# Kernel tuning notes

Measured on AMD Instinct MI355X. Metric: run time of the kernel, lower is better.

## Reference

```python
import jax, jax.numpy as jnp
import numpy as np

N, E, D, H, C = 50000, 250000, 300, 4, 75  # nodes, edges, in_size=300, heads=4, out=75 (H*C=300)


def setup_inputs() -> dict:
    key = jax.random.key(0)
    ks = jax.random.split(key, 32)
    rn = lambda k, shape, s=0.05: jax.random.normal(k, shape, jnp.float32) * s
    inp = {}
    inp['x'] = rn(ks[0], (N, D), 1.0)
    inp['edge_index'] = jax.random.randint(ks[1], (2, E), 0, N, dtype=jnp.int32)
    inp['edge_attr'] = rn(ks[2], (E, 4), 1.0)
    inp['obj_normals'] = rn(ks[3], (N, 3), 1.0)
    # parameters (Linear stored as [in, out] so y = x @ W + b)
    inp['Wq'] = rn(ks[4], (D, H * C)); inp['bq'] = rn(ks[5], (H * C,))
    inp['Wk'] = rn(ks[6], (D, H * C)); inp['bk'] = rn(ks[7], (H * C,))
    inp['Wv'] = rn(ks[8], (D, H * C)); inp['bv'] = rn(ks[9], (H * C,))
    inp['We'] = rn(ks[10], (D, H * C))               # lin_edge, no bias
    inp['Wn'] = rn(ks[11], (3, D)); inp['bn'] = rn(ks[12], (D,))      # map_normal
    inp['Wxy'] = rn(ks[13], (2, D)); inp['bxy'] = rn(ks[14], (D,))    # map_xy_relative_coord
    inp['Wloc'] = rn(ks[15], (3 * D, D)); inp['bloc'] = rn(ks[16], (D,))  # map_back_edge_loc
    inp['Wobj'] = rn(ks[17], (2 * D, D)); inp['bobj'] = rn(ks[18], (D,))  # map_back_edge_obj
    inp['Wfus'] = rn(ks[19], (2 * D, D)); inp['bfus'] = rn(ks[20], (D,))  # hv_words_fusion
    inp['Wcls'] = rn(ks[21], (D, 5)); inp['bcls'] = rn(ks[22], (5,))      # horizontal_word_cls
    inp['Wskip'] = rn(ks[23], (D, H * C)); inp['bskip'] = rn(ks[24], (H * C,))  # lin_skip
    inp['vocab'] = rn(ks[25], (7, D), 1.0)  # spatial_vocab_we
    return inp


def reference(x, edge_index, edge_attr, obj_normals,
              Wq, bq, Wk, bk, Wv, bv, We, Wn, bn, Wxy, bxy,
              Wloc, bloc, Wobj, bobj, Wfus, bfus, Wcls, bcls,
              Wskip, bskip, vocab):
    src, dst = edge_index[0], edge_index[1]  # x_j = x[src], x_i = x[dst]
    x_i = x[dst]
    x_j = x[src]
    q = (x_i @ Wq + bq).reshape(E, H, C)
    k = (x_j @ Wk + bk).reshape(E, H, C)
    # vertical (top/bottom) word embeddings gated by edge_attr signs
    top = (edge_attr[:, 0] > 0).astype(x.dtype)[:, None] * vocab[0][None, :]
    bot = (edge_attr[:, 1] < 0).astype(x.dtype)[:, None] * vocab[1][None, :]
    vert = top + bot                                           # [E, D]
    # horizontal word probabilities from geometry + feature cues
    ni = obj_normals[dst] @ Wn + bn
    nj = obj_normals[src] @ Wn + bn
    xy = edge_attr[:, 2:4] @ Wxy + bxy
    loc = jnp.concatenate([xy, ni, nj], axis=1) @ Wloc + bloc
    obj = jnp.concatenate([x_i, x_j - x_i], axis=1) @ Wobj + bobj
    prob = jax.nn.softmax(jnp.tanh(obj + loc) @ Wcls + bcls, axis=1)   # [E, 5]
    horiz = prob @ vocab[2:7]                                  # [E, D]
    edge_word = jnp.concatenate([vert, horiz], axis=1) @ Wfus + bfus   # [E, D]
    ef = (edge_word @ We).reshape(E, H, C)                     # lin_edge
    k = k + ef
    # scaled dot-product attention with per-destination-node softmax
    alpha = (q * k).sum(-1) / jnp.asarray(np.sqrt(C), x.dtype)  # [E, H]
    m = jax.ops.segment_max(alpha, dst, num_segments=N)
    alpha = jnp.exp(alpha - m[dst])
    den = jax.ops.segment_sum(alpha, dst, num_segments=N)
    alpha = alpha / den[dst]
    v = (x_j @ Wv + bv).reshape(E, H, C) + ef
    msg = v * alpha[..., None]                                  # [E, H, C]
    out = jax.ops.segment_sum(msg, dst, num_segments=N).reshape(N, H * C)
    out = out + x @ Wskip + bskip                               # concat heads + root skip
    return out
```

## Files before the change

kernel.cpp:

```cpp
#include <hip/hip_runtime.h>
#include <hip/hip_bf16.h>
#include <math.h>

#define NDIM 300
#define KPAD 320
#define NREAL 1800
#define NPAD 1920

typedef __hip_bfloat16 bf16;
typedef __attribute__((ext_vector_type(8))) short short8;
typedef __attribute__((ext_vector_type(4))) float f32x4;

__device__ __forceinline__ void gl_lds16(const void* g, void* l) {
    __builtin_amdgcn_global_load_lds(
        (const __attribute__((address_space(1))) void*)g,
        (__attribute__((address_space(3))) void*)l, 16, 0, 0);
}

__device__ __forceinline__ float bflo(uint u) { return __uint_as_float(u << 16); }
__device__ __forceinline__ float bfhi(uint u) { return __uint_as_float(u & 0xFFFF0000u); }

__global__ void k1_pre_conv_hist(
    const float* __restrict__ Wn, const float* __restrict__ bn,
    const float* __restrict__ Wxy, const float* __restrict__ bxy,
    const float* __restrict__ Wloc, const float* __restrict__ bloc,
    const float* __restrict__ bobj,
    const float* __restrict__ Wfus,
    const float* __restrict__ vocab,
    float* __restrict__ Wn1, float* __restrict__ Wn2,
    float* __restrict__ Mxy, float* __restrict__ bgeo,
    float* __restrict__ vf5, float* __restrict__ t0, float* __restrict__ t1,
    const float* __restrict__ X, const float* __restrict__ Nrm,
    bf16* __restrict__ Xb, int M, int nconv,
    const int* __restrict__ ei, int* __restrict__ deg, int E)
{
    const int bid = blockIdx.x;
    if (bid < 19) {
        int i = bid * 256 + threadIdx.x;
        if (i < 900) {
            int r = i / 300, c = i % 300;
            float s = 0.f;
            for (int k = 0; k < 300; k++) s += Wn[r*300+k] * Wloc[(300+k)*300+c];
            Wn1[i] = s;
        } else if (i < 1800) {
            int j = i - 900; int r = j/300, c = j%300;
            float s = 0.f;
            for (int k = 0; k < 300; k++) s += Wn[r*300+k] * Wloc[(600+k)*300+c];
            Wn2[j] = s;
        } else if (i < 2400) {
            int j = i - 1800; int r = j/300, c = j%300;
            float s = 0.f;
            for (int k = 0; k < 300; k++) s += Wxy[r*300+k] * Wloc[k*300+c];
            Mxy[j] = 2.f * s;
        } else if (i < 2700) {
            int c = i - 2400;
            float s = bloc[c] + bobj[c];
            for (int k = 0; k < 300; k++) s += bxy[k] * Wloc[k*300+c];
            for (int k = 0; k < 300; k++) s += bn[k] * (Wloc[(300+k)*300+c] + Wloc[(600+k)*300+c]);
            bgeo[c] = 2.f * s;
        } else if (i < 4200) {
            int j = i - 2700; int p = j/300, c = j%300;
            float s = 0.f;
            for (int k = 0; k < 300; k++) s += vocab[(2+p)*300+k] * Wfus[(300+k)*300+c];
            vf5[j] = s;
        } else if (i < 4500) {
            int c = i - 4200;
            float s = 0.f;
            for (int k = 0; k < 300; k++) s += vocab[k] * Wfus[k*300+c];
            t0[c] = s;
        } else if (i < 4800) {
            int c = i - 4500;
            float s = 0.f;
            for (int k = 0; k < 300; k++) s += vocab[300+k] * Wfus[k*300+c];
            t1[c] = s;
        }
    } else if (bid < 19 + nconv) {
        int i = (bid - 19) * 256 + threadIdx.x;
        int row = i / 40, c8 = i % 40;
        if (row >= M) return;
        int c0 = c8 * 8;
        union { bf16 h[8]; short8 s; } u;
        #pragma unroll
        for (int t = 0; t < 8; t++) {
            int c = c0 + t;
            float v = 0.f;
            if (c < 300)      v = X[(size_t)row * 300 + c];
            else if (c < 303) v = Nrm[(size_t)row * 3 + (c - 300)];
            u.h[t] = __float2bfloat16(v);
        }
        *(short8*)&Xb[(size_t)row * 320 + c0] = u.s;
    } else {
        int e = (bid - 19 - nconv) * 256 + threadIdx.x;
        if (e < E) atomicAdd(&deg[ei[E + e]], 1);
    }
}

__global__ void k2_pre2_pack(
    const float* __restrict__ We, const float* __restrict__ bfus,
    const float* __restrict__ vf5, const float* __restrict__ t0, const float* __restrict__ t1,
    const float* __restrict__ Wcls,
    float* __restrict__ E8, float* __restrict__ WclsT,
    const float* __restrict__ Wq, const float* __restrict__ Wk,
    const float* __restrict__ Wv, const float* __restrict__ Wskip,
    const float* __restrict__ Wobj,
    const float* __restrict__ Wn1, const float* __restrict__ Wn2,
    const float* __restrict__ bq, const float* __restrict__ bk,
    const float* __restrict__ bv, const float* __restrict__ bskip,
    bf16* __restrict__ WcatT, float* __restrict__ bcat)
{
    const int bid = blockIdx.x;
    if (bid < 16) {
        int i = bid * 256 + threadIdx.x;
        if (i < 2400) {
            int r = i / 300, c = i % 300;
            const float* src;
            if (r == 0) src = t0;
            else if (r == 1) src = t1;
            else if (r == 7) src = bfus;
            else src = vf5 + (r - 2) * 300;
            float s = 0.f;
            for (int k = 0; k < 300; k++) s += src[k] * We[k*300+c];
            E8[i] = s;
        } else if (i < 3900) {
            int j = i - 2400; int cl = j / 300, c = j % 300;
            WclsT[cl * 300 + c] = Wcls[c * 5 + cl];
        }
    } else {
        int i = (bid - 16) * 256 + threadIdx.x;
        if (i < NREAL) {
            int c = i;
            float b = 0.f;
            if (c < 600)       { if (!(c & 1)) b = bq[c >> 1]; }
            else if (c < 1200) { int cc = c - 600; if (cc & 1) b = bk[cc >> 1]; }
            else if (c < 1500) b = bv[c - 1200];
            else               b = bskip[c - 1500];
            bcat[i] = b;
        }
        if (i < NPAD * KPAD) {
            int cp = i / KPAD, k = i % KPAD;
            float v = 0.f;
            if (cp < NREAL) {
                int seg, jj;
                if (cp < 600)       { jj = cp >> 1; seg = (cp & 1) ? 4 : 0; }
                else if (cp < 1200) { int cc = cp - 600; jj = cc >> 1; seg = (cc & 1) ? 1 : 5; }
                else if (cp < 1500) { jj = cp - 1200; seg = 2; }
                else                { jj = cp - 1500; seg = 3; }
                if (k < 300) {
                    switch (seg) {
                        case 0: v = Wq[k*300+jj]; break;
                        case 1: v = Wk[k*300+jj]; break;
                        case 2: v = Wv[k*300+jj]; break;
                        case 3: v = Wskip[k*300+jj]; break;
                        case 4: v = Wobj[k*300+jj] - Wobj[(300+k)*300+jj]; break;
                        default: v = Wobj[(300+k)*300+jj]; break;
                    }
                } else if (k < 303) {
                    if (seg == 4) v = Wn1[(k-300)*300+jj];
                    else if (seg == 5) v = Wn2[(k-300)*300+jj];
                }
                if (seg >= 4) v *= 2.f;
            }
            WcatT[i] = __float2bfloat16(v);
        }
    }
}

__global__ __launch_bounds__(1024) void scan_local(
    const int* __restrict__ deg, int* __restrict__ off, int* __restrict__ bsum, int N)
{
    __shared__ int buf[1024];
    int i = blockIdx.x * 1024 + threadIdx.x;
    int v = (i < N) ? deg[i] : 0;
    buf[threadIdx.x] = v;
    __syncthreads();
    #pragma unroll
    for (int ofs = 1; ofs < 1024; ofs <<= 1) {
        int t = (threadIdx.x >= ofs) ? buf[threadIdx.x - ofs] : 0;
        __syncthreads();
        buf[threadIdx.x] += t;
        __syncthreads();
    }
    if (i < N) off[i] = buf[threadIdx.x] - v;
    if (threadIdx.x == 1023) bsum[blockIdx.x] = buf[1023];
}

__global__ __launch_bounds__(1024) void scan_bsum(
    const int* __restrict__ bsum, int* __restrict__ bexc, int nb)
{
    __shared__ int buf[1024];
    int v = (threadIdx.x < nb) ? bsum[threadIdx.x] : 0;
    buf[threadIdx.x] = v;
    __syncthreads();
    #pragma unroll
    for (int ofs = 1; ofs < 1024; ofs <<= 1) {
        int t = (threadIdx.x >= ofs) ? buf[threadIdx.x - ofs] : 0;
        __syncthreads();
        buf[threadIdx.x] += t;
        __syncthreads();
    }
    if (threadIdx.x < nb) bexc[threadIdx.x] = buf[threadIdx.x] - v;
}

__global__ void scan_add(int* __restrict__ off, int* __restrict__ cur,
                         const int* __restrict__ bexc, int N, int E)
{
    int i = blockIdx.x * blockDim.x + threadIdx.x;
    if (i < N) {
        int o = off[i] + bexc[i >> 10];
        off[i] = o; cur[i] = o;
    }
    if (i == 0) off[N] = E;
}

__global__ __launch_bounds__(256) void gemm_mfma(
    const bf16* __restrict__ Xb,
    const bf16* __restrict__ Bt, const float* __restrict__ bcat,
    bf16* __restrict__ QP, bf16* __restrict__ PK, bf16* __restrict__ V,
    float* __restrict__ Ot, int M, int npan)
{
    __shared__ __align__(16) char smraw[32768];
    bf16*  Asb = (bf16*)smraw;
    bf16*  Bsb = (bf16*)(smraw + 16384);
    bf16*  EP  = (bf16*)smraw;
    float* EPf = (float*)smraw;

    const int bid = blockIdx.x;
    int p, cx;
    {
        const int full = (npan >> 3) * 120;
        if (bid < full) {
            int g = bid / 120, r = bid - g * 120;
            p = (g << 3) + (r & 7); cx = r >> 3;
        } else {
            int r = bid - full;
            int tp = npan & 7;
            p = (npan & ~7) + r % tp; cx = r / tp;
        }
    }
    const int r0 = p * 128;
    const int c0 = cx * 128;

    const int tid  = threadIdx.x;
    const int wave = tid >> 6;
    const int lane = tid & 63;
    const int wm = (wave >> 1) * 64;
    const int wn = (wave & 1) * 64;
    const int lr = lane & 15;
    const int lq = lane >> 4;

    f32x4 acc[4][4];
    #pragma unroll
    for (int j = 0; j < 4; j++)
        #pragma unroll
        for (int i = 0; i < 4; i++) acc[j][i] = (f32x4){0.f, 0.f, 0.f, 0.f};

    const bf16* aSrc[2];
    const bf16* bSrc[2];
    {
        const int bcol_l = lane >> 2;
        const int bkp    = (lane & 3) * 8;
        #pragma unroll
        for (int h = 0; h < 2; h++) {
            int t = h * 256 + wave * 64 + lane;
            int grow = min(r0 + (t >> 2), M - 1);
            aSrc[h] = Xb + (size_t)grow * 320 + (t & 3) * 8;
            bSrc[h] = Bt + (size_t)(c0 + wave * 32 + h * 16 + bcol_l) * KPAD + bkp;
        }
    }

    auto stage = [&](int buf, int kb) {
        #pragma unroll
        for (int h = 0; h < 2; h++) {
            int tbase = h * 256 + wave * 64;
            gl_lds16(aSrc[h] + kb, &Asb[buf * 4096 + tbase * 8]);
        }
        #pragma unroll
        for (int h = 0; h < 2; h++) {
            int cloc = wave * 32 + h * 16;
            gl_lds16(bSrc[h] + kb, &Bsb[buf * 4096 + cloc * 32]);
        }
    };

    stage(0, 0);
    #pragma unroll
    for (int it = 0; it < 10; it++) {
        __syncthreads();
        if (it < 9) stage((it + 1) & 1, (it + 1) * 32);
        const int b = it & 1;
        short8 af[4], bfr[4];
        #pragma unroll
        for (int i = 0; i < 4; i++)
            af[i] = *(const short8*)&Asb[b * 4096 + (wm + i * 16 + lr) * 32 + lq * 8];
        #pragma unroll
        for (int j = 0; j < 4; j++)
            bfr[j] = *(const short8*)&Bsb[b * 4096 + (wn + j * 16 + lr) * 32 + lq * 8];
        #pragma unroll
        for (int j = 0; j < 4; j++)
            #pragma unroll
            for (int i = 0; i < 4; i++)
                acc[j][i] = __builtin_amdgcn_mfma_f32_16x16x32_bf16(
                    bfr[j], af[i], acc[j][i], 0, 0, 0);
    }

    if (c0 < 1500) {
        #pragma unroll
        for (int hm = 0; hm < 2; hm++) {
            __syncthreads();
            if ((wave >> 1) == hm) {
                #pragma unroll
                for (int j = 0; j < 4; j++) {
                    int colL = wn + j * 16 + lq * 4;
                    float4 bb = *(const float4*)&bcat[c0 + colL];
                    #pragma unroll
                    for (int i = 0; i < 4; i++) {
                        int row = i * 16 + lr;
                        union { bf16 h[4]; uint2 u2; } pk;
                        pk.h[0] = __float2bfloat16(acc[j][i][0] + bb.x);
                        pk.h[1] = __float2bfloat16(acc[j][i][1] + bb.y);
                        pk.h[2] = __float2bfloat16(acc[j][i][2] + bb.z);
                        pk.h[3] = __float2bfloat16(acc[j][i][3] + bb.w);
                        *(uint2*)&EP[row * 136 + colL] = pk.u2;
                    }
                }
            }
            __syncthreads();
            #pragma unroll
            for (int rep = 0; rep < 8; rep++) {
                int row = wave * 16 + rep * 2 + (lane >> 5);
                int gr = r0 + hm * 64 + row;
                int col = c0 + 4 * (lane & 31);
                if (gr < M && col < 1500) {
                    uint2 val = *(const uint2*)&EP[row * 136 + 4 * (lane & 31)];
                    if (col < 600)       *(uint2*)&QP[(size_t)gr * 600 + col] = val;
                    else if (col < 1200) *(uint2*)&PK[(size_t)gr * 600 + (col - 600)] = val;
                    else                 *(uint2*)&V [(size_t)gr * 300 + (col - 1200)] = val;
                }
            }
        }
    }
    if (c0 + 128 > 1500) {
        #pragma unroll
        for (int hm = 0; hm < 2; hm++) {
            #pragma unroll
            for (int h = 0; h < 2; h++) {
                if (c0 + h * 64 + 63 < 1500) continue;
                __syncthreads();
                if ((wave >> 1) == hm && (wave & 1) == h) {
                    #pragma unroll
                    for (int j = 0; j < 4; j++) {
                        int colL = j * 16 + lq * 4;
                        int colb = c0 + h * 64 + colL;
                        if (colb < NREAL) {
                            float4 bb = *(const float4*)&bcat[colb];
                            #pragma unroll
                            for (int i = 0; i < 4; i++) {
                                int row = i * 16 + lr;
                                f32x4 vv;
                                vv[0] = acc[j][i][0] + bb.x;
                                vv[1] = acc[j][i][1] + bb.y;
                                vv[2] = acc[j][i][2] + bb.z;
                                vv[3] = acc[j][i][3] + bb.w;
                                *(f32x4*)&EPf[row * 68 + colL] = vv;
                            }
                        }
                    }
                }
                __syncthreads();
                #pragma unroll
                for (int rep = 0; rep < 16; rep++) {
                    int row = wave * 16 + rep;
                    int gr = r0 + hm * 64 + row;
                    int col = c0 + h * 64 + lane;
                    if (gr < M && col >= 1500 && col < NREAL)
                        Ot[(size_t)gr * 300 + (col - 1500)] = EPf[row * 68 + lane];
                }
            }
        }
    }
}

__global__ __launch_bounds__(256) void k3_scatter_qe8(
    const int* __restrict__ ei, const float* __restrict__ ea,
    int* __restrict__ cur,
    int2* __restrict__ esd, float* __restrict__ eas, int E, int ebk,
    const bf16* __restrict__ QP, const float* __restrict__ E8,
    float* __restrict__ QE8f, int N)
{
    __shared__ unsigned short Qs[64 * 302];
    const int bid = blockIdx.x;
    if (bid < ebk) {
        int e = bid * 256 + threadIdx.x;
        if (e < E) {
            int s = ei[e];
            int d = ei[E + e];
            float4 a = *(const float4*)&ea[(size_t)e * 4];
            int p = atomicAdd(&cur[d], 1);
            esd[p] = make_int2(s, d);
            *(float4*)&eas[(size_t)p * 4] = a;
        }
        return;
    }
    const int tid = threadIdx.x;
    const int n0 = (bid - ebk) * 64;
    const int nrows = min(64, N - n0);
    const int nu = nrows * 300;
    const uint* src = (const uint*)QP + (size_t)n0 * 300;
    for (int i = tid; i < nu; i += 256) {
        int rr = i / 300, cc = i - rr * 300;
        Qs[rr * 302 + cc] = (unsigned short)src[i];
    }
    __syncthreads();
    const int w = tid >> 6, l = tid & 63;
    if (l >= nrows) return;
    float acc[8] = {0.f,0.f,0.f,0.f,0.f,0.f,0.f,0.f};
    const int cb = 75 * w;
    for (int cc = 0; cc < 75; cc++) {
        int c = cb + cc;
        float qv = __uint_as_float(((uint)Qs[l * 302 + c]) << 16);
        #pragma unroll
        for (int s = 0; s < 8; s++) acc[s] += qv * E8[s * 300 + c];
    }
    float* out = QE8f + (size_t)(n0 + l) * 32;
    #pragma unroll
    for (int s = 0; s < 8; s++) out[s * 4 + w] = acc[s];
}

__global__ __launch_bounds__(256) void edge_alpha(
    const int2* __restrict__ esd, const float* __restrict__ eas,
    const bf16* __restrict__ QP, const bf16* __restrict__ PK,
    const float* __restrict__ Mxy, const float* __restrict__ bgeo,
    const float* __restrict__ QE8f, const float* __restrict__ WclsT,
    const float* __restrict__ bcls,
    float* __restrict__ AW,
    int E, int nwaves)
{
    __shared__ __align__(16) float red[4][20 * 68];
    __shared__ float res[4][20];
    const int wv   = threadIdx.x >> 6;
    const int lane = threadIdx.x & 63;
    float* __restrict__ rw = red[wv];
    float* __restrict__ rs = res[wv];
    const int gw  = blockIdx.x * 4 + wv;
    const int per = (E + nwaves - 1) / nwaves;
    const int t0  = gw * per;
    if (t0 >= E) return;
    const int t1 = min(t0 + per, E);
    const bool ok4 = lane < 44;

    float mx0[5], mx1[5], bg[5], wcl[5][5];
    #pragma unroll
    for (int r = 0; r < 4; r++) {
        int c = lane + 64 * r;
        mx0[r] = Mxy[c]; mx1[r] = Mxy[300 + c]; bg[r] = bgeo[c];
        #pragma unroll
        for (int cl = 0; cl < 5; cl++) wcl[cl][r] = WclsT[cl * 300 + c];
    }
    {
        int c = lane + 256;
        mx0[4] = ok4 ? Mxy[c] : 0.f;
        mx1[4] = ok4 ? Mxy[300 + c] : 0.f;
        bg[4]  = ok4 ? bgeo[c] : 0.f;
        #pragma unroll
        for (int cl = 0; cl < 5; cl++) wcl[cl][4] = ok4 ? WclsT[cl * 300 + c] : 0.f;
    }
    float bc[5];
    #pragma unroll
    for (int cl = 0; cl < 5; cl++) bc[cl] = bcls[cl];
    const float isc = 0.11547005383792516f;

    const uint* QPu = (const uint*)QP;
    const uint* PKu = (const uint*)PK;

    int prev_d = -1;
    float qv[5], pib[5];
    float prt[18];

    auto reload = [&](int dd) {
        const uint* qr = QPu + (size_t)dd * 300 + lane;
        #pragma unroll
        for (int r = 0; r < 4; r++) {
            uint uq = qr[64 * r];
            qv[r] = bflo(uq); pib[r] = bfhi(uq) + bg[r];
        }
        uint uq = ok4 ? qr[256] : 0u;
        qv[4] = bflo(uq); pib[4] = bfhi(uq) + bg[4];
    };
    auto compute = [&](const uint (&pk)[5], float az, float aw_, int ub) {
        float tt[5], qk[5];
        #pragma unroll
        for (int r = 0; r < 5; r++) {
            float pj = bflo(pk[r]), kf = bfhi(pk[r]);
            float v = pib[r] + pj + az * mx0[r] + aw_ * mx1[r];
            tt[r] = fmaf(-2.f, __builtin_amdgcn_rcpf(1.f + __expf(v)), 1.f);
            qk[r] = qv[r] * kf;
        }
        #pragma unroll
        for (int cl = 0; cl < 5; cl++)
            prt[ub + cl] = tt[0]*wcl[cl][0] + tt[1]*wcl[cl][1] + tt[2]*wcl[cl][2]
                         + tt[3]*wcl[cl][3] + tt[4]*wcl[cl][4];
        float h0 = qk[0], h3 = qk[4], h1 = 0.f, h2 = 0.f;
        if (lane < 11) h0 += qk[1]; else h1 += qk[1];
        if (lane < 22) h1 += qk[2]; else h2 += qk[2];
        if (lane < 33) h2 += qk[3]; else h3 += qk[3];
        prt[ub+5] = h0; prt[ub+6] = h1; prt[ub+7] = h2; prt[ub+8] = h3;
    };

    for (int t = t0; t < t1; t += 2) {
        const int i0 = t;
        const int i1 = (t + 1 < t1) ? t + 1 : t;
        const int2 sd0 = esd[i0], sd1 = esd[i1];
        const float4 a40 = *(const float4*)&eas[(size_t)4 * i0];
        const float4 a41 = *(const float4*)&eas[(size_t)4 * i1];

        uint pk0[5], pk1[5];
        const uint* p0r = PKu + (size_t)sd0.x * 300 + lane;
        const uint* p1r = PKu + (size_t)sd1.x * 300 + lane;
        #pragma unroll
        for (int r = 0; r < 4; r++) { pk0[r] = p0r[64 * r]; pk1[r] = p1r[64 * r]; }
        pk0[4] = ok4 ? p0r[256] : 0u;
        pk1[4] = ok4 ? p1r[256] : 0u;

        if (sd0.y != prev_d) reload(sd0.y);
        compute(pk0, a40.z, a40.w, 0);
        if (sd1.y != sd0.y) reload(sd1.y);
        compute(pk1, a41.z, a41.w, 9);
        prev_d = sd1.y;

        #pragma unroll
        for (int v = 0; v < 18; v++) rw[v * 68 + lane] = prt[v];
        #pragma unroll
        for (int i = 0; i < 5; i++) {
            int v = 4 * i + (lane >> 4);
            const f32x4 q4 = *(const f32x4*)&rw[v * 68 + (lane & 15) * 4];
            float s = (q4[0] + q4[1]) + (q4[2] + q4[3]);
            s += __shfl_xor(s, 1, 64);
            s += __shfl_xor(s, 2, 64);
            s += __shfl_xor(s, 4, 64);
            s += __shfl_xor(s, 8, 64);
            if ((lane & 15) == 0 && v < 18) rs[v] = s;
        }
        {
            const int    u  = lane >> 5;
            const int    ub = u * 9;
            const float4 au = u ? a41 : a40;
            const int    dd = u ? sd1.y : sd0.y;
            const int    tw = u ? i1 : i0;
            float lg0 = rs[ub+0] + bc[0], lg1 = rs[ub+1] + bc[1], lg2 = rs[ub+2] + bc[2];
            float lg3 = rs[ub+3] + bc[3], lg4 = rs[ub+4] + bc[4];
            float mxv = fmaxf(fmaxf(fmaxf(lg0, lg1), fmaxf(lg2, lg3)), lg4);
            float p0 = __expf(lg0 - mxv), p1 = __expf(lg1 - mxv), p2 = __expf(lg2 - mxv);
            float p3 = __expf(lg3 - mxv), p4 = __expf(lg4 - mxv);
            float pinv = __builtin_amdgcn_rcpf(p0 + p1 + p2 + p3 + p4);
            p0 *= pinv; p1 *= pinv; p2 *= pinv; p3 *= pinv; p4 *= pinv;
            float ct  = au.x > 0.f ? 1.f : 0.f;
            float cb_ = au.y < 0.f ? 1.f : 0.f;
            const f32x4* qe = (const f32x4*)(QE8f + (size_t)dd * 32);
            f32x4 addv = ct*qe[0] + cb_*qe[1] + p0*qe[2] + p1*qe[3]
                       + p2*qe[4] + p3*qe[5] + p4*qe[6] + qe[7];
            float ax0 = __expf((rs[ub+5] + addv[0]) * isc);
            float ax1 = __expf((rs[ub+6] + addv[1]) * isc);
            float ax2 = __expf((rs[ub+7] + addv[2]) * isc);
            float ax3 = __expf((rs[ub+8] + addv[3]) * isc);
            if ((lane & 31) == 0) {
                float* awp = AW + (size_t)12 * tw;
                *(float4*)(awp)     = make_float4(ax0, ax1, ax2, ax3);
                *(float4*)(awp + 4) = make_float4(ct, cb_, p0, p1);
                *(float4*)(awp + 8) = make_float4(p2, p3, p4, 0.f);
            }
        }
    }
}

__global__ __launch_bounds__(256) void node_pv(
    const int2* __restrict__ esd, const bf16* __restrict__ V,
    const float* __restrict__ E8, const float* __restrict__ AW,
    const int* __restrict__ off,
    float* __restrict__ Ot, int N)
{
    const int wid  = threadIdx.x >> 6;
    const int lane = threadIdx.x & 63;
    const int n = blockIdx.x * 4 + wid;
    if (n >= N) return;
    const int e0 = off[n], e1 = off[n + 1];
    if (e0 == e1) return;
    const size_t nrow = (size_t)n * 300;
    const bool ok4 = lane < 44;

    float e8r[8][5];
    #pragma unroll
    for (int rr = 0; rr < 8; rr++) {
        #pragma unroll
        for (int r = 0; r < 4; r++) e8r[rr][r] = E8[rr * 300 + lane + 64 * r];
        e8r[rr][4] = ok4 ? E8[rr * 300 + lane + 256] : 0.f;
    }

    float macc[5] = {0.f, 0.f, 0.f, 0.f, 0.f};
    float den0 = 0.f, den1 = 0.f, den2 = 0.f, den3 = 0.f;

    int t = e0;
    for (; t + 4 <= e1; t += 4) {
        int s4[4];
        #pragma unroll
        for (int u = 0; u < 4; u++) s4[u] = esd[t + u].x;
        float vv[4][5];
        #pragma unroll
        for (int u = 0; u < 4; u++) {
            const bf16* vr = V + (size_t)s4[u] * 300 + lane;
            #pragma unroll
            for (int r = 0; r < 4; r++) vv[u][r] = __bfloat162float(vr[64 * r]);
            vv[u][4] = ok4 ? __bfloat162float(vr[256]) : 0.f;
        }
        #pragma unroll
        for (int u = 0; u < 4; u++) {
            const float* awp = AW + (size_t)12 * (t + u);
            float4 ax = *(const float4*)(awp);
            float4 wa = *(const float4*)(awp + 4);
            float4 wb = *(const float4*)(awp + 8);
            #pragma unroll
            for (int r = 0; r < 5; r++) {
                float efc = wa.x * e8r[0][r] + wa.y * e8r[1][r] + wa.z * e8r[2][r]
                          + wa.w * e8r[3][r] + wb.x * e8r[4][r] + wb.y * e8r[5][r]
                          + wb.z * e8r[6][r] + e8r[7][r];
                float w = (r == 0) ? ax.x
                        : (r == 1) ? (lane < 11 ? ax.x : ax.y)
                        : (r == 2) ? (lane < 22 ? ax.y : ax.z)
                        : (r == 3) ? (lane < 33 ? ax.z : ax.w)
                        : ax.w;
                macc[r] += w * (vv[u][r] + efc);
            }
            den0 += ax.x; den1 += ax.y; den2 += ax.z; den3 += ax.w;
        }
    }
    for (; t < e1; t++) {
        int s = esd[t].x;
        const float* awp = AW + (size_t)12 * t;
        float4 ax = *(const float4*)(awp);
        float4 wa = *(const float4*)(awp + 4);
        float4 wb = *(const float4*)(awp + 8);
        const bf16* vr = V + (size_t)s * 300 + lane;
        #pragma unroll
        for (int r = 0; r < 5; r++) {
            float vvs = (r < 4) ? __bfloat162float(vr[64 * r])
                                : (ok4 ? __bfloat162float(vr[256]) : 0.f);
            float efc = wa.x * e8r[0][r] + wa.y * e8r[1][r] + wa.z * e8r[2][r]
                      + wa.w * e8r[3][r] + wb.x * e8r[4][r] + wb.y * e8r[5][r]
                      + wb.z * e8r[6][r] + e8r[7][r];
            float w = (r == 0) ? ax.x
                    : (r == 1) ? (lane < 11 ? ax.x : ax.y)
                    : (r == 2) ? (lane < 22 ? ax.y : ax.z)
                    : (r == 3) ? (lane < 33 ? ax.z : ax.w)
                    : ax.w;
            macc[r] += w * (vvs + efc);
        }
        den0 += ax.x; den1 += ax.y; den2 += ax.z; den3 += ax.w;
    }

    const float rd0 = __builtin_amdgcn_rcpf(den0);
    const float rd1 = __builtin_amdgcn_rcpf(den1);
    const float rd2 = __builtin_amdgcn_rcpf(den2);
    const float rd3 = __builtin_amdgcn_rcpf(den3);
    #pragma unroll
    for (int r = 0; r < 5; r++) {
        int c = lane + 64 * r;
        if (c < 300) {
            float rd = (r == 0) ? rd0
                     : (r == 1) ? (lane < 11 ? rd0 : rd1)
                     : (r == 2) ? (lane < 22 ? rd1 : rd2)
                     : (r == 3) ? (lane < 33 ? rd2 : rd3)
                     : rd3;
            Ot[nrow + c] += macc[r] * rd;
        }
    }
}

extern "C" void kernel_launch(void* const* d_in, const int* in_sizes, int n_in,
                              void* d_out, int out_size, void* d_ws, size_t ws_size,
                              hipStream_t stream)
{
    const float* x     = (const float*)d_in[0];
    const int*   ei    = (const int*)  d_in[1];
    const float* ea    = (const float*)d_in[2];
    const float* on    = (const float*)d_in[3];
    const float* Wq    = (const float*)d_in[4];
    const float* bq    = (const float*)d_in[5];
    const float* Wk    = (const float*)d_in[6];
    const float* bk    = (const float*)d_in[7];
    const float* Wv    = (const float*)d_in[8];
    const float* bv    = (const float*)d_in[9];
    const float* We    = (const float*)d_in[10];
    const float* Wn    = (const float*)d_in[11];
    const float* bn    = (const float*)d_in[12];
    const float* Wxy   = (const float*)d_in[13];
    const float* bxy   = (const float*)d_in[14];
    const float* Wloc  = (const float*)d_in[15];
    const float* bloc  = (const float*)d_in[16];
    const float* Wobj  = (const float*)d_in[17];
    const float* bobj  = (const float*)d_in[18];
    const float* Wfus  = (const float*)d_in[19];
    const float* bfus  = (const float*)d_in[20];
    const float* Wcls  = (const float*)d_in[21];
    const float* bcls  = (const float*)d_in[22];
    const float* Wskip = (const float*)d_in[23];
    const float* bskip = (const float*)d_in[24];
    const float* vocab = (const float*)d_in[25];

    const int N = in_sizes[0] / NDIM;
    const int E = in_sizes[1] / 2;

    const size_t nodeElems = (size_t)N * 300;
    const size_t wcatElems = (size_t)NPAD * KPAD;
    const size_t xbElems   = (size_t)N * 320;
    size_t xbBytes = xbElems * sizeof(bf16);
    const size_t ovlBytes = ((size_t)16 * E + (size_t)32 * N) * sizeof(float);
    if (ovlBytes > xbBytes) xbBytes = ovlBytes;

    const size_t f32Elems  = NREAL + 904 + 904 + 600 + 304 + 1504 + 304 + 304 + 2400 + 1504;
    const size_t intElems  = (size_t)N + (size_t)(N + 1) + (size_t)N
                           + (size_t)2 * E + 2048;
    size_t need = (5 * nodeElems + wcatElems) * sizeof(bf16) + xbBytes
                + f32Elems * sizeof(float) + intElems * sizeof(int);
    if (ws_size < need) return;

    bf16* wsh = (bf16*)d_ws;
    bf16* QPb   = wsh;
    bf16* PKb   = QPb + (size_t)2 * nodeElems;
    bf16* Vb    = PKb + (size_t)2 * nodeElems;
    bf16* WcatT = Vb + nodeElems;
    bf16* Xb    = WcatT + wcatElems;
    float* AW   = (float*)Xb;
    float* eas  = AW + (size_t)12 * E;
    float* QE8f = eas + (size_t)4 * E;
    float* ws = (float*)((char*)Xb + xbBytes);
    size_t o = 0;
    float* bcat  = ws + o; o += NREAL;
    float* Wn1   = ws + o; o += 904;
    float* Wn2   = ws + o; o += 904;
    float* Mxyb  = ws + o; o += 600;
    float* bgeo  = ws + o; o += 304;
    float* vf5   = ws + o; o += 1504;
    float* t0b   = ws + o; o += 304;
    float* t1b   = ws + o; o += 304;
    float* E8b   = ws + o; o += 2400;
    float* WclsT = ws + o; o += 1504;
    int* ip = (int*)(ws + o);
    int* deg    = ip;             ip += N;
    int* offb   = ip;             ip += N + 1;
    int* curb   = ip;             ip += N;
    int2* esd   = (int2*)ip;      ip += (size_t)2 * E;
    int* bsum   = ip;             ip += 1024;
    int* bexc   = ip;             ip += 1024;
    (void)n_in; (void)out_size;

    hipMemsetAsync(deg, 0, (size_t)N * sizeof(int), stream);

    const int ebk   = (E + 255) / 256;
    const int nconv = ((int)((size_t)N * 40) + 255) / 256;

    k1_pre_conv_hist<<<19 + nconv + ebk, 256, 0, stream>>>(
        Wn, bn, Wxy, bxy, Wloc, bloc, bobj, Wfus, vocab,
        Wn1, Wn2, Mxyb, bgeo, vf5, t0b, t1b,
        x, on, Xb, N, nconv, ei, deg, E);
    k2_pre2_pack<<<16 + (NPAD * KPAD + 255) / 256, 256, 0, stream>>>(
        We, bfus, vf5, t0b, t1b, Wcls, E8b, WclsT,
        Wq, Wk, Wv, Wskip, Wobj, Wn1, Wn2, bq, bk, bv, bskip, WcatT, bcat);

    const int nbl = (N + 1023) / 1024;
    scan_local<<<nbl, 1024, 0, stream>>>(deg, offb, bsum, N);
    scan_bsum<<<1, 1024, 0, stream>>>(bsum, bexc, nbl);
    scan_add<<<(N + 255) / 256, 256, 0, stream>>>(offb, curb, bexc, N, E);

    const int npan = (N + 127) / 128;
    gemm_mfma<<<npan * 15, 256, 0, stream>>>(Xb, WcatT, bcat,
                                             QPb, PKb, Vb, (float*)d_out, N, npan);

    k3_scatter_qe8<<<ebk + (N + 63) / 64, 256, 0, stream>>>(
        ei, ea, curb, esd, eas, E, ebk, QPb, E8b, QE8f, N);

    const int eab = 2048;
    edge_alpha<<<eab, 256, 0, stream>>>(esd, eas, QPb, PKb,
                                        Mxyb, bgeo, QE8f, WclsT, bcls,
                                        AW, E, eab * 4);

    const int nb = (N + 3) / 4;
    node_pv<<<nb, 256, 0, stream>>>(esd, Vb, E8b, AW,
                                    offb, (float*)d_out, N);
}
```

Baseline: 618.7 us.

## Fuse edge attention and node aggregation into one destination-partitioned kernel

Merges the per-edge alpha kernel and the per-node PV aggregation kernel into one kernel. Each wave binary-searches the CSR offsets to own a contiguous range of destination nodes, computes the attention weights for their edges and accumulates V messages at once. Per-edge weights pass through LDS instead of a global AW buffer, which removes a global write/read round trip and a kernel launch. Work balance now follows node boundaries, so skewed degree distributions can leave some waves with more edges, and a node spanning a chunk boundary is handled entirely by one wave.

```diff
diff --git a/kernel.cpp b/kernel.cpp
--- a/kernel.cpp
+++ b/kernel.cpp
@@ -425,35 +425,49 @@
     for (int s = 0; s < 8; s++) out[s * 4 + w] = acc[s];
 }
 
-__global__ __launch_bounds__(256) void edge_alpha(
+__global__ __launch_bounds__(256) void edge_fused(
     const int2* __restrict__ esd, const float* __restrict__ eas,
     const bf16* __restrict__ QP, const bf16* __restrict__ PK,
+    const bf16* __restrict__ V,
     const float* __restrict__ Mxy, const float* __restrict__ bgeo,
     const float* __restrict__ QE8f, const float* __restrict__ WclsT,
-    const float* __restrict__ bcls,
-    float* __restrict__ AW,
-    int E, int nwaves)
-{
-    __shared__ __align__(16) float red[4][20 * 68];
+    const float* __restrict__ bcls, const float* __restrict__ E8,
+    const int* __restrict__ off,
+    float* __restrict__ Ot, int N, int E, int nwaves)
+{
+    __shared__ __align__(16) float red[4][18 * 68];
     __shared__ float res[4][20];
+    __shared__ __align__(16) float ews[4][2][12];
     const int wv   = threadIdx.x >> 6;
     const int lane = threadIdx.x & 63;
     float* __restrict__ rw = red[wv];
     float* __restrict__ rs = res[wv];
+    float* __restrict__ ew = &ews[wv][0][0];
     const int gw  = blockIdx.x * 4 + wv;
     const int per = (E + nwaves - 1) / nwaves;
-    const int t0  = gw * per;
-    if (t0 >= E) return;
-    const int t1 = min(t0 + per, E);
+    const int lo  = gw * per;
+    if (lo >= E) return;
+    const int hi = min(lo + per, E);
+    int n0, n1;
+    {
+        int a = 0, b = N;
+        while (a < b) { int m = (a + b) >> 1; if (off[m] < lo) a = m + 1; else b = m; }
+        n0 = a; b = N;
+        while (a < b) { int m = (a + b) >> 1; if (off[m] < hi) a = m + 1; else b = m; }
+        n1 = a;
+    }
+    if (n0 >= n1) return;
     const bool ok4 = lane < 44;
 
-    float mx0[5], mx1[5], bg[5], wcl[5][5];
+    float mx0[5], mx1[5], bg[5], wcl[5][5], e8r[8][5];
     #pragma unroll
     for (int r = 0; r < 4; r++) {
         int c = lane + 64 * r;
         mx0[r] = Mxy[c]; mx1[r] = Mxy[300 + c]; bg[r] = bgeo[c];
         #pragma unroll
         for (int cl = 0; cl < 5; cl++) wcl[cl][r] = WclsT[cl * 300 + c];
+        #pragma unroll
+        for (int rr = 0; rr < 8; rr++) e8r[rr][r] = E8[rr * 300 + c];
     }
     {
         int c = lane + 256;
@@ -462,6 +476,8 @@
         bg[4]  = ok4 ? bgeo[c] : 0.f;
         #pragma unroll
         for (int cl = 0; cl < 5; cl++) wcl[cl][4] = ok4 ? WclsT[cl * 300 + c] : 0.f;
+        #pragma unroll
+        for (int rr = 0; rr < 8; rr++) e8r[rr][4] = ok4 ? E8[rr * 300 + c] : 0.f;
     }
     float bc[5];
     #pragma unroll
@@ -470,22 +486,10 @@
 
     const uint* QPu = (const uint*)QP;
     const uint* PKu = (const uint*)PK;
-
-    int prev_d = -1;
-    float qv[5], pib[5];
     float prt[18];
 
-    auto reload = [&](int dd) {
-        const uint* qr = QPu + (size_t)dd * 300 + lane;
-        #pragma unroll
-        for (int r = 0; r < 4; r++) {
-            uint uq = qr[64 * r];
-            qv[r] = bflo(uq); pib[r] = bfhi(uq) + bg[r];
-        }
-        uint uq = ok4 ? qr[256] : 0u;
-        qv[4] = bflo(uq); pib[4] = bfhi(uq) + bg[4];
-    };
-    auto compute = [&](const uint (&pk)[5], float az, float aw_, int ub) {
+    auto compute = [&](const uint (&pk)[5], const float (&qv)[5], const float (&pib)[5],
+                       float az, float aw_, int ub) {
         float tt[5], qk[5];
         #pragma unroll
         for (int r = 0; r < 5; r++) {
@@ -505,170 +509,134 @@
         prt[ub+5] = h0; prt[ub+6] = h1; prt[ub+7] = h2; prt[ub+8] = h3;
     };
 
-    for (int t = t0; t < t1; t += 2) {
-        const int i0 = t;
-        const int i1 = (t + 1 < t1) ? t + 1 : t;
-        const int2 sd0 = esd[i0], sd1 = esd[i1];
-        const float4 a40 = *(const float4*)&eas[(size_t)4 * i0];
-        const float4 a41 = *(const float4*)&eas[(size_t)4 * i1];
-
-        uint pk0[5], pk1[5];
-        const uint* p0r = PKu + (size_t)sd0.x * 300 + lane;
-        const uint* p1r = PKu + (size_t)sd1.x * 300 + lane;
-        #pragma unroll
-        for (int r = 0; r < 4; r++) { pk0[r] = p0r[64 * r]; pk1[r] = p1r[64 * r]; }
-        pk0[4] = ok4 ? p0r[256] : 0u;
-        pk1[4] = ok4 ? p1r[256] : 0u;
-
-        if (sd0.y != prev_d) reload(sd0.y);
-        compute(pk0, a40.z, a40.w, 0);
-        if (sd1.y != sd0.y) reload(sd1.y);
-        compute(pk1, a41.z, a41.w, 9);
-        prev_d = sd1.y;
-
-        #pragma unroll
-        for (int v = 0; v < 18; v++) rw[v * 68 + lane] = prt[v];
-        #pragma unroll
-        for (int i = 0; i < 5; i++) {
-            int v = 4 * i + (lane >> 4);
-            const f32x4 q4 = *(const f32x4*)&rw[v * 68 + (lane & 15) * 4];
-            float s = (q4[0] + q4[1]) + (q4[2] + q4[3]);
-            s += __shfl_xor(s, 1, 64);
-            s += __shfl_xor(s, 2, 64);
-            s += __shfl_xor(s, 4, 64);
-            s += __shfl_xor(s, 8, 64);
-            if ((lane & 15) == 0 && v < 18) rs[v] = s;
-        }
+    for (int n = n0; n < n1; n++) {
+        const int e0 = off[n], e1 = off[n + 1];
+        if (e0 == e1) continue;
+        float qv[5], pib[5];
         {
-            const int    u  = lane >> 5;
-            const int    ub = u * 9;
-            const float4 au = u ? a41 : a40;
-            const int    dd = u ? sd1.y : sd0.y;
-            const int    tw = u ? i1 : i0;
-            float lg0 = rs[ub+0] + bc[0], lg1 = rs[ub+1] + bc[1], lg2 = rs[ub+2] + bc[2];
-            float lg3 = rs[ub+3] + bc[3], lg4 = rs[ub+4] + bc[4];
-            float mxv = fmaxf(fmaxf(fmaxf(lg0, lg1), fmaxf(lg2, lg3)), lg4);
-            float p0 = __expf(lg0 - mxv), p1 = __expf(lg1 - mxv), p2 = __expf(lg2 - mxv);
-            float p3 = __expf(lg3 - mxv), p4 = __expf(lg4 - mxv);
-            float pinv = __builtin_amdgcn_rcpf(p0 + p1 + p2 + p3 + p4);
-            p0 *= pinv; p1 *= pinv; p2 *= pinv; p3 *= pinv; p4 *= pinv;
-            float ct  = au.x > 0.f ? 1.f : 0.f;
-            float cb_ = au.y < 0.f ? 1.f : 0.f;
-            const f32x4* qe = (const f32x4*)(QE8f + (size_t)dd * 32);
-            f32x4 addv = ct*qe[0] + cb_*qe[1] + p0*qe[2] + p1*qe[3]
-                       + p2*qe[4] + p3*qe[5] + p4*qe[6] + qe[7];
-            float ax0 = __expf((rs[ub+5] + addv[0]) * isc);
-            float ax1 = __expf((rs[ub+6] + addv[1]) * isc);
-            float ax2 = __expf((rs[ub+7] + addv[2]) * isc);
-            float ax3 = __expf((rs[ub+8] + addv[3]) * isc);
-            if ((lane & 31) == 0) {
-                float* awp = AW + (size_t)12 * tw;
-                *(float4*)(awp)     = make_float4(ax0, ax1, ax2, ax3);
-                *(float4*)(awp + 4) = make_float4(ct, cb_, p0, p1);
-                *(float4*)(awp + 8) = make_float4(p2, p3, p4, 0.f);
-            }
-        }
-    }
-}
-
-__global__ __launch_bounds__(256) void node_pv(
-    const int2* __restrict__ esd, const bf16* __restrict__ V,
-    const float* __restrict__ E8, const float* __restrict__ AW,
-    const int* __restrict__ off,
-    float* __restrict__ Ot, int N)
-{
-    const int wid  = threadIdx.x >> 6;
-    const int lane = threadIdx.x & 63;
-    const int n = blockIdx.x * 4 + wid;
-    if (n >= N) return;
-    const int e0 = off[n], e1 = off[n + 1];
-    if (e0 == e1) return;
-    const size_t nrow = (size_t)n * 300;
-    const bool ok4 = lane < 44;
-
-    float e8r[8][5];
-    #pragma unroll
-    for (int rr = 0; rr < 8; rr++) {
-        #pragma unroll
-        for (int r = 0; r < 4; r++) e8r[rr][r] = E8[rr * 300 + lane + 64 * r];
-        e8r[rr][4] = ok4 ? E8[rr * 300 + lane + 256] : 0.f;
-    }
-
-    float macc[5] = {0.f, 0.f, 0.f, 0.f, 0.f};
-    float den0 = 0.f, den1 = 0.f, den2 = 0.f, den3 = 0.f;
-
-    int t = e0;
-    for (; t + 4 <= e1; t += 4) {
-        int s4[4];
-        #pragma unroll
-        for (int u = 0; u < 4; u++) s4[u] = esd[t + u].x;
-        float vv[4][5];
-        #pragma unroll
-        for (int u = 0; u < 4; u++) {
-            const bf16* vr = V + (size_t)s4[u] * 300 + lane;
+            const uint* qr = QPu + (size_t)n * 300 + lane;
             #pragma unroll
-            for (int r = 0; r < 4; r++) vv[u][r] = __bfloat162float(vr[64 * r]);
-            vv[u][4] = ok4 ? __bfloat162float(vr[256]) : 0.f;
-        }
-        #pragma unroll
-        for (int u = 0; u < 4; u++) {
-            const float* awp = AW + (size_t)12 * (t + u);
-            float4 ax = *(const float4*)(awp);
-            float4 wa = *(const float4*)(awp + 4);
-            float4 wb = *(const float4*)(awp + 8);
+            for (int r = 0; r < 4; r++) {
+                uint uq = qr[64 * r];
+                qv[r] = bflo(uq); pib[r] = bfhi(uq) + bg[r];
+            }
+            uint uq = ok4 ? qr[256] : 0u;
+            qv[4] = bflo(uq); pib[4] = bfhi(uq) + bg[4];
+        }
+        const f32x4* qe = (const f32x4*)(QE8f + (size_t)n * 32);
+        float macc[5] = {0.f, 0.f, 0.f, 0.f, 0.f};
+        float den0 = 0.f, den1 = 0.f, den2 = 0.f, den3 = 0.f;
+
+        for (int t = e0; t < e1; t += 2) {
+            const int i0 = t;
+            const bool has1 = (t + 1 < e1);
+            const int i1 = has1 ? t + 1 : t;
+            const int s0 = esd[i0].x, s1 = esd[i1].x;
+            const float4 a40 = *(const float4*)&eas[(size_t)4 * i0];
+            const float4 a41 = *(const float4*)&eas[(size_t)4 * i1];
+
+            uint pk0[5], pk1[5];
+            const uint* p0r = PKu + (size_t)s0 * 300 + lane;
+            const uint* p1r = PKu + (size_t)s1 * 300 + lane;
             #pragma unroll
-            for (int r = 0; r < 5; r++) {
-                float efc = wa.x * e8r[0][r] + wa.y * e8r[1][r] + wa.z * e8r[2][r]
-                          + wa.w * e8r[3][r] + wb.x * e8r[4][r] + wb.y * e8r[5][r]
-                          + wb.z * e8r[6][r] + e8r[7][r];
-                float w = (r == 0) ? ax.x
-                        : (r == 1) ? (lane < 11 ? ax.x : ax.y)
-                        : (r == 2) ? (lane < 22 ? ax.y : ax.z)
-                        : (r == 3) ? (lane < 33 ? ax.z : ax.w)
-                        : ax.w;
-                macc[r] += w * (vv[u][r] + efc);
-            }
-            den0 += ax.x; den1 += ax.y; den2 += ax.z; den3 += ax.w;
-        }
-    }
-    for (; t < e1; t++) {
-        int s = esd[t].x;
-        const float* awp = AW + (size_t)12 * t;
-        float4 ax = *(const float4*)(awp);
-        float4 wa = *(const float4*)(awp + 4);
-        float4 wb = *(const float4*)(awp + 8);
-        const bf16* vr = V + (size_t)s * 300 + lane;
+            for (int r = 0; r < 4; r++) { pk0[r] = p0r[64 * r]; pk1[r] = p1r[64 * r]; }
+            pk0[4] = ok4 ? p0r[256] : 0u;
+            pk1[4] = ok4 ? p1r[256] : 0u;
+
+            compute(pk0, qv, pib, a40.z, a40.w, 0);
+            compute(pk1, qv, pib, a41.z, a41.w, 9);
+
+            #pragma unroll
+            for (int v = 0; v < 18; v++) rw[v * 68 + lane] = prt[v];
+            #pragma unroll
+            for (int i = 0; i < 5; i++) {
+                int v = 4 * i + (lane >> 4);
+                const f32x4 q4 = *(const f32x4*)&rw[v * 68 + (lane & 15) * 4];
+                float s = (q4[0] + q4[1]) + (q4[2] + q4[3]);
+                s += __shfl_xor(s, 1, 64);
+                s += __shfl_xor(s, 2, 64);
+                s += __shfl_xor(s, 4, 64);
+                s += __shfl_xor(s, 8, 64);
+                if ((lane & 15) == 0 && v < 18) rs[v] = s;
+            }
+            {
+                const int    u  = lane >> 5;
+                const int    ub = u * 9;
+                const float4 au = u ? a41 : a40;
+                float lg0 = rs[ub+0] + bc[0], lg1 = rs[ub+1] + bc[1], lg2 = rs[ub+2] + bc[2];
+                float lg3 = rs[ub+3] + bc[3], lg4 = rs[ub+4] + bc[4];
+                float mxv = fmaxf(fmaxf(fmaxf(lg0, lg1), fmaxf(lg2, lg3)), lg4);
+                float p0 = __expf(lg0 - mxv), p1 = __expf(lg1 - mxv), p2 = __expf(lg2 - mxv);
+                float p3 = __expf(lg3 - mxv), p4 = __expf(lg4 - mxv);
+                float pinv = __builtin_amdgcn_rcpf(p0 + p1 + p2 + p3 + p4);
+                p0 *= pinv; p1 *= pinv; p2 *= pinv; p3 *= pinv; p4 *= pinv;
+                float ct  = au.x > 0.f ? 1.f : 0.f;
+                float cb_ = au.y < 0.f ? 1.f : 0.f;
+                f32x4 addv = ct*qe[0] + cb_*qe[1] + p0*qe[2] + p1*qe[3]
+                           + p2*qe[4] + p3*qe[5] + p4*qe[6] + qe[7];
+                float ax0 = __expf((rs[ub+5] + addv[0]) * isc);
+                float ax1 = __expf((rs[ub+6] + addv[1]) * isc);
+                float ax2 = __expf((rs[ub+7] + addv[2]) * isc);
+                float ax3 = __expf((rs[ub+8] + addv[3]) * isc);
+                if ((lane & 31) == 0) {
+                    float* ewp = ew + u * 12;
+                    *(float4*)(ewp)     = make_float4(ax0, ax1, ax2, ax3);
+                    *(float4*)(ewp + 4) = make_float4(ct, cb_, p0, p1);
+                    *(float4*)(ewp + 8) = make_float4(p2, p3, p4, 0.f);
+                }
+            }
+            float vv0[5], vv1[5];
+            {
+                const bf16* v0r = V + (size_t)s0 * 300 + lane;
+                const bf16* v1r = V + (size_t)s1 * 300 + lane;
+                #pragma unroll
+                for (int r = 0; r < 4; r++) {
+                    vv0[r] = __bfloat162float(v0r[64 * r]);
+                    vv1[r] = __bfloat162float(v1r[64 * r]);
+                }
+                vv0[4] = ok4 ? __bfloat162float(v0r[256]) : 0.f;
+                vv1[4] = ok4 ? __bfloat162float(v1r[256]) : 0.f;
+            }
+            #pragma unroll
+            for (int u = 0; u < 2; u++) {
+                if (u == 1 && !has1) break;
+                const float* ewp = ew + u * 12;
+                float4 ax = *(const float4*)(ewp);
+                float4 wa = *(const float4*)(ewp + 4);
+                float4 wb = *(const float4*)(ewp + 8);
+                const float* vvp = u ? vv1 : vv0;
+                #pragma unroll
+                for (int r = 0; r < 5; r++) {
+                    float efc = wa.x * e8r[0][r] + wa.y * e8r[1][r] + wa.z * e8r[2][r]
+                              + wa.w * e8r[3][r] + wb.x * e8r[4][r] + wb.y * e8r[5][r]
+                              + wb.z * e8r[6][r] + e8r[7][r];
+                    float w = (r == 0) ? ax.x
+                            : (r == 1) ? (lane < 11 ? ax.x : ax.y)
+                            : (r == 2) ? (lane < 22 ? ax.y : ax.z)
+                            : (r == 3) ? (lane < 33 ? ax.z : ax.w)
+                            : ax.w;
+                    macc[r] += w * (vvp[r] + efc);
+                }
+                den0 += ax.x; den1 += ax.y; den2 += ax.z; den3 += ax.w;
+            }
+        }
+
+        const float rd0 = __builtin_amdgcn_rcpf(den0);
+        const float rd1 = __builtin_amdgcn_rcpf(den1);
+        const float rd2 = __builtin_amdgcn_rcpf(den2);
+        const float rd3 = __builtin_amdgcn_rcpf(den3);
+        const size_t nrow = (size_t)n * 300;
         #pragma unroll
         for (int r = 0; r < 5; r++) {
-            float vvs = (r < 4) ? __bfloat162float(vr[64 * r])
-                                : (ok4 ? __bfloat162float(vr[256]) : 0.f);
-            float efc = wa.x * e8r[0][r] + wa.y * e8r[1][r] + wa.z * e8r[2][r]
-                      + wa.w * e8r[3][r] + wb.x * e8r[4][r] + wb.y * e8r[5][r]
-                      + wb.z * e8r[6][r] + e8r[7][r];
-            float w = (r == 0) ? ax.x
-                    : (r == 1) ? (lane < 11 ? ax.x : ax.y)
-                    : (r == 2) ? (lane < 22 ? ax.y : ax.z)
-                    : (r == 3) ? (lane < 33 ? ax.z : ax.w)
-                    : ax.w;
-            macc[r] += w * (vvs + efc);
-        }
-        den0 += ax.x; den1 += ax.y; den2 += ax.z; den3 += ax.w;
-    }
-
-    const float rd0 = __builtin_amdgcn_rcpf(den0);
-    const float rd1 = __builtin_amdgcn_rcpf(den1);
-    const float rd2 = __builtin_amdgcn_rcpf(den2);
-    const float rd3 = __builtin_amdgcn_rcpf(den3);
-    #pragma unroll
-    for (int r = 0; r < 5; r++) {
-        int c = lane + 64 * r;
-        if (c < 300) {
-            float rd = (r == 0) ? rd0
-                     : (r == 1) ? (lane < 11 ? rd0 : rd1)
-                     : (r == 2) ? (lane < 22 ? rd1 : rd2)
-                     : (r == 3) ? (lane < 33 ? rd2 : rd3)
-                     : rd3;
-            Ot[nrow + c] += macc[r] * rd;
+            int c = lane + 64 * r;
+            if (c < 300) {
+                float rd = (r == 0) ? rd0
+                         : (r == 1) ? (lane < 11 ? rd0 : rd1)
+                         : (r == 2) ? (lane < 22 ? rd1 : rd2)
+                         : (r == 3) ? (lane < 33 ? rd2 : rd3)
+                         : rd3;
+                Ot[nrow + c] += macc[r] * rd;
+            }
         }
     }
 }
@@ -749,7 +717,7 @@
     int2* esd   = (int2*)ip;      ip += (size_t)2 * E;
     int* bsum   = ip;             ip += 1024;
     int* bexc   = ip;             ip += 1024;
-    (void)n_in; (void)out_size;
+    (void)n_in; (void)out_size; (void)AW;
 
     hipMemsetAsync(deg, 0, (size_t)N * sizeof(int), stream);
 
@@ -777,11 +745,7 @@
         ei, ea, curb, esd, eas, E, ebk, QPb, E8b, QE8f, N);
 
     const int eab = 2048;
-    edge_alpha<<<eab, 256, 0, stream>>>(esd, eas, QPb, PKb,
-                                        Mxyb, bgeo, QE8f, WclsT, bcls,
-                                        AW, E, eab * 4);
-
-    const int nb = (N + 3) / 4;
-    node_pv<<<nb, 256, 0, stream>>>(esd, Vb, E8b, AW,
-                                    offb, (float*)d_out, N);
-}
+    edge_fused<<<eab, 256, 0, stream>>>(esd, eas, QPb, PKb, Vb,
+                                        Mxyb, bgeo, QE8f, WclsT, bcls, E8b,
+                                        offb, (float*)d_out, N, E, eab * 4);
+}
```

After: 709.3 us. 1.15x slower.
